# Kernel tuning notes

Hardware: AMD Instinct MI355X
Metric: run time of the kernel (lower is better)

The kernel has to match this reference:

```python
import jax, jax.numpy as jnp
import numpy as np

SMOOTH = 1.0
MAX_DIST = 10


def _neighbor_conv(x):
    # 3x3 ones kernel with zero center, padding=1 (NCHW, C=1)
    k = jnp.ones((1, 1, 3, 3), x.dtype).at[0, 0, 1, 1].set(0.0)
    return jax.lax.conv_general_dilated(
        x, k, window_strides=(1, 1), padding=[(1, 1), (1, 1)],
        dimension_numbers=('NCHW', 'OIHW', 'NCHW'))


def _analyze_skeleton(skel):
    n = _neighbor_conv(skel)
    on = skel > 0.5
    endpoints = ((n == 1) & on).astype(skel.dtype)
    midpoints = ((n == 2) & on).astype(skel.dtype)
    junctions = ((n > 2) & on).astype(skel.dtype)
    return endpoints, midpoints, junctions


def _iou(p, g):
    inter = jnp.sum(p * g, axis=(2, 3))
    union = jnp.sum(p, axis=(2, 3)) + jnp.sum(g, axis=(2, 3)) - inter
    return (inter + SMOOTH) / (union + SMOOTH)


def _structural_similarity(pred_skel, gt_skel):
    pe, pm, pj = _analyze_skeleton(pred_skel)
    ge, gm, gj = _analyze_skeleton(gt_skel)
    e_iou, m_iou, j_iou = _iou(pe, ge), _iou(pm, gm), _iou(pj, gj)
    ge_c = jnp.sum(ge, axis=(2, 3))
    gj_c = jnp.sum(gj, axis=(2, 3))
    gm_c = jnp.sum(gm, axis=(2, 3))
    total = ge_c + gj_c + gm_c + SMOOTH
    loss = 1.0 - ((ge_c / total) * e_iou + (gj_c / total) * j_iou + (gm_c / total) * m_iou)
    return loss.mean()


def _maxpool3(x):
    return jax.lax.reduce_window(
        x, -jnp.inf, jax.lax.max,
        window_dimensions=(1, 1, 3, 3), window_strides=(1, 1, 1, 1),
        padding=[(0, 0), (0, 0), (1, 1), (1, 1)])


def _distance_approximation(target, reference):
    # Fixed MAX_DIST iterations; identical math to the torch early-exit loop
    # because new_points requires ~found_mask (no distance is overwritten).
    tgt_on = target > 0.5

    def step(carry, d):
        dilated, found, dist = carry
        dilated = _maxpool3(dilated)
        new = (dilated > 0.5) & tgt_on & (~found)
        dist = dist + d.astype(dist.dtype) * new.astype(dist.dtype)
        return (dilated, found | new, dist), None

    init = (reference, jnp.zeros(target.shape, bool), jnp.zeros_like(target))
    (_, found, dist), _ = jax.lax.scan(step, init, jnp.arange(1, MAX_DIST + 1, dtype=jnp.int32))
    unfound = tgt_on & (~found)
    dist = dist + jnp.asarray(MAX_DIST, dist.dtype) * unfound.astype(dist.dtype)
    total_points = jnp.sum(tgt_on.astype(dist.dtype), axis=(2, 3))
    return jnp.sum(dist, axis=(2, 3)) / (total_points + SMOOTH)


def _medial_axis_distance(pred_skel, gt_skel):
    p2g = _distance_approximation(pred_skel, gt_skel)
    g2p = _distance_approximation(gt_skel, pred_skel)
    return (((p2g + g2p) / 2.0) / MAX_DIST).mean()


def setup_inputs() -> dict:
    key = jax.random.key(0)
    k1, k2 = jax.random.split(key)
    B, C, H, W = 32, 1, 512, 512
    pred_skel = jax.random.uniform(k1, (B, C, H, W), dtype=jnp.float32)
    gt_skel = (jax.random.uniform(k2, (B, C, H, W), dtype=jnp.float32) < 0.1).astype(jnp.float32)
    return {"pred_skel": pred_skel, "gt_skel": gt_skel}


def reference(pred_skel, gt_skel):
    inter = jnp.sum(pred_skel * gt_skel, axis=(2, 3))
    psum = jnp.sum(pred_skel, axis=(2, 3))
    gsum = jnp.sum(gt_skel, axis=(2, 3))
    dice = (2.0 * inter + SMOOTH) / (psum + gsum + SMOOTH)
    dice_loss = 1.0 - dice.mean()
    structural_loss = _structural_similarity(pred_skel, gt_skel)
    medial_loss = _medial_axis_distance(pred_skel, gt_skel)
    avg_mag = (dice_loss + structural_loss + medial_loss) / 3.0
    bal_dice = dice_loss / (dice_loss + SMOOTH) * avg_mag
    bal_struct = structural_loss / (structural_loss + SMOOTH) * avg_mag
    bal_medial = medial_loss / (medial_loss + SMOOTH) * avg_mag
    return bal_dice + bal_struct + bal_medial
```

## Files before the change

### kernel.cpp

```cpp
#include <hip/hip_runtime.h>
#include <stdint.h>

#define BATCH 32
#define H 512
#define W 512
#define NACC 16
#define TH 32
#define HALO 9
#define RH (TH + 2*HALO)
#define NWORDS (RH*8)
#define NT 1024
#define NW (NT/64)
#define NTILE (H/TH)
#define NBLK (NTILE*BATCH)


__global__ __launch_bounds__(NT, 4) void fused_kernel(
    const float* __restrict__ pred, const float* __restrict__ gt,
    float* __restrict__ part)
{
    __shared__ uint64_t MpS[NWORDS + 2];
    __shared__ uint64_t MgS[NWORDS + 2];
    __shared__ float    EC[2][TH];
    __shared__ float    redf[NW][2];
    __shared__ unsigned redu[NW][5];

    uint64_t* Mp = MpS + 1;
    uint64_t* Mg = MgS + 1;

    int fid  = blockIdx.x;
    int b    = fid & 31;
    int tile = fid >> 5;

    const float* pimg = pred + (size_t)b * H * W;
    const float* gimg = gt   + (size_t)b * H * W;
    int y0 = tile * TH;
    int tid = threadIdx.x, lane = tid & 63, wid = tid >> 6;

    float v0 = 0.f, v1 = 0.f;
    for (int s0 = wid; s0 < NWORDS; s0 += 4 * NW) {
        float vp[4], vg[4];
        #pragma unroll
        for (int u = 0; u < 4; ++u) {
            int s = s0 + u * NW;
            vp[u] = 0.f; vg[u] = 0.f;
            int ry = y0 - HALO + (s >> 3);
            if (s < NWORDS && (unsigned)ry < (unsigned)H) {
                int i0 = ry * W + (s & 7) * 64 + lane;
                vp[u] = pimg[i0]; vg[u] = gimg[i0];
            }
        }
        #pragma unroll
        for (int u = 0; u < 4; ++u) {
            int s = s0 + u * NW;
            if (s < NWORDS) {
                unsigned long long mp = __ballot(vp[u] > 0.5f);
                unsigned long long mg = __ballot(vg[u] > 0.5f);
                if (lane == 0) { Mp[s] = mp; Mg[s] = mg; }
                int r = s >> 3;
                if (r >= HALO && r < HALO + TH) {
                    v1 += vp[u];
                    v0 += (vg[u] > 0.5f) ? vp[u] : 0.f;
                }
            }
        }
    }
    if (tid == 0) { MpS[0] = 0; MpS[NWORDS + 1] = 0; MgS[0] = 0; MgS[NWORDS + 1] = 0; }

    bool isStencil = tid >= 512;
    int idx = tid & 511;
    int qi = idx & 127, h2 = idx >> 7;
    int x4 = qi * 4;
    int ys = y0 + h2 * 8;
    float4 pm4 = make_float4(0, 0, 0, 0), pc4 = make_float4(0, 0, 0, 0);
    if (isStencil) {
        if (ys > 0) pm4 = *(const float4*)(pimg + (size_t)(ys - 1) * W + x4);
        pc4 = *(const float4*)(pimg + (size_t)ys * W + x4);
    }

    if (tid < 2 * TH) {
        int c = tid >> 5, r = tid & (TH - 1);
        int y = y0 + r, col = 255 + c;
        float sum = (y > 0     ? pimg[(size_t)(y - 1) * W + col] : 0.f)
                  +              pimg[(size_t)y * W + col]
                  + (y < H - 1 ? pimg[(size_t)(y + 1) * W + col] : 0.f);
        EC[c][r] = sum;
    }
    __syncthreads();

    uint64_t cpack = 0ULL;
    int dsum = 0, dcnt = 0;

    if (isStencil) {
        int wdx = qi >> 4;
        int ss = (qi & 15) * 4;
        auto win6 = [&](int rb) -> uint32_t {
            const uint64_t* row = &Mg[rb * 8];
            uint64_t bm = row[wdx];
            if (ss == 0) {
                uint64_t lo = wdx ? row[wdx - 1] : 0ULL;
                return (uint32_t)(((bm << 1) | (lo >> 63)) & 0x3FULL);
            }
            uint32_t v = (uint32_t)((bm >> (ss - 1)) & 0x3FULL);
            if (ss == 60) {
                uint64_t hi = (wdx < 7) ? row[wdx + 1] : 0ULL;
                v |= ((uint32_t)hi & 1u) << 5;
            }
            return v;
        };
        int rb0 = h2 * 8 + HALO - 1;
        uint32_t wU = win6(rb0), wM = win6(rb0 + 1);

        for (int r = 0; r < 8; ++r) {
            int y = ys + r;
            float4 pp4 = (y < H - 1) ? *(const float4*)(pimg + (size_t)(y + 1) * W + x4)
                                     : make_float4(0, 0, 0, 0);
            uint32_t wD = win6(rb0 + 2 + r);
            int ry = h2 * 8 + r;

            float ps[6];
            ps[1] = pm4.x + pc4.x + pp4.x; ps[2] = pm4.y + pc4.y + pp4.y;
            ps[3] = pm4.z + pc4.z + pp4.z; ps[4] = pm4.w + pc4.w + pp4.w;
            float psl = __shfl_up(ps[4], 1, 64);
            float psr = __shfl_down(ps[1], 1, 64);
            if (lane == 0)  psl = (qi == 0)   ? 0.f : EC[0][ry];
            if (lane == 63) psr = (qi == 127) ? 0.f : EC[1][ry];
            ps[0] = psl; ps[5] = psr;

            float pcv[4] = {pc4.x, pc4.y, pc4.z, pc4.w};
            #pragma unroll
            for (int j = 0; j < 4; ++j) {
                float np = ps[j] + ps[j + 1] + ps[j + 2] - pcv[j];
                bool pon = pcv[j] > 0.5f;
                bool pe  = pon && (np == 1.f);
                bool pmb = pon && (np == 2.f);
                bool pjb = pon && (np > 2.f);
                uint32_t n9 = ((wU >> j) & 7u) | (((wM >> j) & 7u) << 3) | (((wD >> j) & 7u) << 6);
                uint32_t cen = (wM >> (j + 1)) & 1u;
                int ng = __popc(n9) - (int)cen;
                bool gon = cen != 0u;
                bool ge  = gon && (ng == 1);
                bool gmb = gon && (ng == 2);
                bool gjb = gon && (ng > 2);
                cpack += (uint64_t)pe
                       | ((uint64_t)pmb << 7)
                       | ((uint64_t)pjb << 14)
                       | ((uint64_t)ge  << 21)
                       | ((uint64_t)gmb << 28)
                       | ((uint64_t)gjb << 35)
                       | ((uint64_t)(pe  && ge)  << 42)
                       | ((uint64_t)(pmb && gmb) << 49)
                       | ((uint64_t)(pjb && gjb) << 56);
            }
            pm4 = pc4; pc4 = pp4; wU = wM; wM = wD;
        }
    } else {
        bool isP = tid < 256;
        int di = tid & 255;
        int o  = (HALO + (di >> 3)) * 8 + (di & 7);
        int w  = di & 7;
        bool wL = (w > 0), wR = (w < 7);
        const uint64_t* MT = isP ? Mp : Mg;
        const uint64_t* MV = isP ? Mg : Mp;

        uint64_t T = MT[o];
        dcnt = __popcll(T);
        dsum = dcnt;
        uint64_t VM = MV[o];
        uint64_t VL = wL ? MV[o - 1] : 0ULL;
        uint64_t VR = wR ? MV[o + 1] : 0ULL;
        uint64_t C = VM;

        #pragma unroll
        for (int a = 1; a <= 9; ++a) {
            int lo = o - 8 * a, hi = o + 8 * a;
            uint64_t NM = MV[lo] | MV[hi];
            uint64_t NL = wL ? (MV[lo - 1] | MV[hi - 1]) : 0ULL;
            uint64_t NR = wR ? (MV[lo + 1] | MV[hi + 1]) : 0ULL;
            uint64_t SL = NL, SM = NM, SR = NR;
            const int m = a - 1;
            if (m >= 1) {
                SM |= (SM << 1) | (SM >> 1) | (SL >> 63) | (SR << 63);
                SL |= SL << 1; SR |= SR >> 1;
            }
            if (m >= 2) {
                const int s = (m == 2) ? 1 : 2;
                SM |= (SM << s) | (SM >> s) | (SL >> (64 - s)) | (SR << (64 - s));
                SL |= SL << s; SR |= SR >> s;
            }
            if (m >= 4) {
                const int s = (m - 3 < 4) ? (m - 3) : 4;
                SM |= (SM << s) | (SM >> s) | (SL >> (64 - s)) | (SR << (64 - s));
                SL |= SL << s; SR |= SR >> s;
            }
            if (m >= 8) {
                const int s = m - 7;
                SM |= (SM << s) | (SM >> s) | (SL >> (64 - s)) | (SR << (64 - s));
                SL |= SL << s; SR |= SR >> s;
            }
            C |= SM;
            VL |= NL; VM |= NM; VR |= NR;
            C |= (VM << a) | (VM >> a) | (VL >> (64 - a)) | (VR << (64 - a));
            dsum += __popcll(T & ~C);
        }
    }

    unsigned r0, r1, r2, r3, r4;
    if (isStencil) {
        unsigned c3  = (unsigned)( cpack        & 0x7F);
        unsigned c4  = (unsigned)((cpack >> 7 ) & 0x7F);
        unsigned c5  = (unsigned)((cpack >> 14) & 0x7F);
        unsigned c6  = (unsigned)((cpack >> 21) & 0x7F);
        unsigned c7  = (unsigned)((cpack >> 28) & 0x7F);
        unsigned c8  = (unsigned)((cpack >> 35) & 0x7F);
        unsigned c9  = (unsigned)((cpack >> 42) & 0x7F);
        unsigned c10 = (unsigned)((cpack >> 49) & 0x7F);
        unsigned c11 = (unsigned)((cpack >> 56) & 0x7F);
        r0 = c3 | (c4 << 16); r1 = c5 | (c6 << 16); r2 = c7 | (c8 << 16);
        r3 = c9 | (c10 << 16); r4 = c11;
    } else {
        r0 = (unsigned)dsum | ((unsigned)dcnt << 16);
        r1 = 0; r2 = 0; r3 = 0; r4 = 0;
    }
    #pragma unroll
    for (int off = 32; off; off >>= 1) {
        v0 += __shfl_down(v0, off, 64);
        v1 += __shfl_down(v1, off, 64);
        r0 += __shfl_down(r0, off, 64);
        r1 += __shfl_down(r1, off, 64);
        r2 += __shfl_down(r2, off, 64);
        r3 += __shfl_down(r3, off, 64);
        r4 += __shfl_down(r4, off, 64);
    }
    if (lane == 0) {
        redf[wid][0] = v0; redf[wid][1] = v1;
        redu[wid][0] = r0; redu[wid][1] = r1; redu[wid][2] = r2;
        redu[wid][3] = r3; redu[wid][4] = r4;
    }
    __syncthreads();
    if (tid < 16) {
        int k = tid;
        float s = 0.f;
        if (k < 2) {
            #pragma unroll
            for (int wv = 0; wv < NW; ++wv) s += redf[wv][k];
        } else if (k == 2) {
            unsigned u = 0;
            for (int wv = 4; wv < 8; ++wv) u += redu[wv][0] >> 16;
            s = (float)u;
        } else if (k <= 10) {
            int pair = (k - 3) >> 1, hi = (k - 3) & 1;
            unsigned u = 0;
            for (int wv = 8; wv < 16; ++wv) u += (redu[wv][pair] >> (hi * 16)) & 0xFFFFu;
            s = (float)u;
        } else if (k == 11) {
            unsigned u = 0;
            for (int wv = 8; wv < 16; ++wv) u += redu[wv][4];
            s = (float)u;
        } else {
            int base = (k < 14) ? 0 : 4, hi = k & 1;
            unsigned u = 0;
            for (int wv = base; wv < base + 4; ++wv)
                u += (redu[wv][0] >> (hi * 16)) & 0xFFFFu;
            s = (float)u;
        }
        part[fid * NACC + k] = s;
    }
}

__global__ __launch_bounds__(512) void final_kernel(
    const float* __restrict__ part, float* __restrict__ out)
{
    __shared__ float sacc[BATCH][NACC];
    __shared__ float tri[BATCH][3];
    int t = threadIdx.x;
    {
        int b = t >> 4, k = t & 15;
        float s = 0.f;
        #pragma unroll 4
        for (int j = 0; j < NTILE; ++j)
            s += part[((j << 5) + b) * NACC + k];
        sacc[b][k] = s;
    }
    __syncthreads();
    if (t < BATCH) {
        const float* a = sacc[t];
        float inter = a[0], psum = a[1], gsum = a[2];
        float dice = (2.f * inter + 1.f) / (psum + gsum + 1.f);

        float pe = a[3], pm = a[4], pj = a[5];
        float ge = a[6], gm = a[7], gj = a[8];
        float ie = a[9], im = a[10], ij = a[11];
        float e_iou = (ie + 1.f) / (pe + ge - ie + 1.f);
        float m_iou = (im + 1.f) / (pm + gm - im + 1.f);
        float j_iou = (ij + 1.f) / (pj + gj - ij + 1.f);
        float total = ge + gj + gm + 1.f;
        float sloss = 1.f - ((ge / total) * e_iou + (gj / total) * j_iou + (gm / total) * m_iou);

        float p2g = a[12] / (a[13] + 1.f);
        float g2p = a[14] / (a[15] + 1.f);
        float med = ((p2g + g2p) * 0.5f) / 10.f;
        tri[t][0] = dice; tri[t][1] = sloss; tri[t][2] = med;
    }
    __syncthreads();
    if (t == 0) {
        float dice = 0.f, sloss = 0.f, med = 0.f;
        for (int b = 0; b < BATCH; ++b) {
            dice += tri[b][0]; sloss += tri[b][1]; med += tri[b][2];
        }
        float dice_loss  = 1.f - dice / (float)BATCH;
        float structural = sloss / (float)BATCH;
        float medial     = med / (float)BATCH;
        float avg = (dice_loss + structural + medial) / 3.f;
        float r = dice_loss  / (dice_loss  + 1.f) * avg
                + structural / (structural + 1.f) * avg
                + medial     / (medial     + 1.f) * avg;
        out[0] = r;
    }
}

extern "C" void kernel_launch(void* const* d_in, const int* in_sizes, int n_in,
                              void* d_out, int out_size, void* d_ws, size_t ws_size,
                              hipStream_t stream)
{
    const float* pred = (const float*)d_in[0];
    const float* gt   = (const float*)d_in[1];
    float* part = (float*)d_ws;
    float* out  = (float*)d_out;

    fused_kernel<<<dim3(NBLK), NT, 0, stream>>>(pred, gt, part);
    final_kernel<<<1, 512, 0, stream>>>(part, out);
}
```

Measured before the change: 118.8 us.

## Classify GT skeleton with bit-sliced popcount in LDS and early-exit distance loop

Computes the ground-truth endpoint/midpoint/junction masks once per tile using a bit-parallel carry-save adder over 64-bit packed rows, stores them in shared memory, and has stencil threads read single bits instead of recomputing per-pixel 3x3 popcounts. The GT counts move to the distance-threads' reduction slot, which cuts the packed reduction from five registers to three. The distance dilation loop now exits once a wavefront has no remaining unfound target bits. This adds shared memory and one extra barrier in exchange for less per-pixel integer work and fewer dilation iterations.

```diff
diff --git a/kernel.cpp b/kernel.cpp
--- a/kernel.cpp
+++ b/kernel.cpp
@@ -21,9 +21,12 @@
 {
     __shared__ uint64_t MpS[NWORDS + 2];
     __shared__ uint64_t MgS[NWORDS + 2];
+    __shared__ uint64_t Ge[TH * 8];
+    __shared__ uint64_t Gm[TH * 8];
+    __shared__ uint64_t Gj[TH * 8];
     __shared__ float    EC[2][TH];
     __shared__ float    redf[NW][2];
-    __shared__ unsigned redu[NW][5];
+    __shared__ unsigned redu[NW][3];
 
     uint64_t* Mp = MpS + 1;
     uint64_t* Mg = MgS + 1;
@@ -88,35 +91,53 @@
     }
     __syncthreads();
 
+    unsigned cge = 0, cgm = 0, cgj = 0;
+    if (tid < 256) {
+        int r = tid >> 3, w = tid & 7;
+        int oM = (HALO + r) * 8 + w;
+        bool wl = (w > 0), wr = (w < 7);
+        uint64_t A  = Mg[oM - 8], Bm = Mg[oM], Cm = Mg[oM + 8];
+        uint64_t AL = wl ? Mg[oM - 9] : 0ULL, AR = wr ? Mg[oM - 7] : 0ULL;
+        uint64_t BL = wl ? Mg[oM - 1] : 0ULL, BR = wr ? Mg[oM + 1] : 0ULL;
+        uint64_t CL = wl ? Mg[oM + 7] : 0ULL, CR = wr ? Mg[oM + 9] : 0ULL;
+        uint64_t Aw = (A  << 1) | (AL >> 63), Ae = (A  >> 1) | (AR << 63);
+        uint64_t Bw = (Bm << 1) | (BL >> 63), Be = (Bm >> 1) | (BR << 63);
+        uint64_t Cw = (Cm << 1) | (CL >> 63), Ce = (Cm >> 1) | (CR << 63);
+        uint64_t c1, c2, c3, c5;
+        uint64_t t;
+        t = Aw ^ A;  uint64_t s1 = t ^ Ae;  c1 = (Aw & A)  | (Ae & t);
+        t = Bw ^ Be; uint64_t s2 = t ^ Cw;  c2 = (Bw & Be) | (Cw & t);
+        t = Cm ^ Ce; uint64_t s3 = t ^ s1;  c3 = (Cm & Ce) | (s1 & t);
+        uint64_t b0 = s2 ^ s3, c4 = s2 & s3;
+        t = c1 ^ c2; uint64_t s5 = t ^ c3;  c5 = (c1 & c2) | (c3 & t);
+        uint64_t b1 = s5 ^ c4, c6 = s5 & c4;
+        uint64_t b2 = c5 ^ c6, b3 = c5 & c6;
+        uint64_t nz23 = ~(b2 | b3);
+        uint64_t ge = Bm & b0 & ~b1 & nz23;
+        uint64_t gm = Bm & b1 & ~b0 & nz23;
+        uint64_t gj = Bm & (b2 | b3 | (b1 & b0));
+        Ge[tid] = ge; Gm[tid] = gm; Gj[tid] = gj;
+        cge = (unsigned)__popcll(ge);
+        cgm = (unsigned)__popcll(gm);
+        cgj = (unsigned)__popcll(gj);
+    }
+    __syncthreads();
+
     uint64_t cpack = 0ULL;
     int dsum = 0, dcnt = 0;
 
     if (isStencil) {
         int wdx = qi >> 4;
         int ss = (qi & 15) * 4;
-        auto win6 = [&](int rb) -> uint32_t {
-            const uint64_t* row = &Mg[rb * 8];
-            uint64_t bm = row[wdx];
-            if (ss == 0) {
-                uint64_t lo = wdx ? row[wdx - 1] : 0ULL;
-                return (uint32_t)(((bm << 1) | (lo >> 63)) & 0x3FULL);
-            }
-            uint32_t v = (uint32_t)((bm >> (ss - 1)) & 0x3FULL);
-            if (ss == 60) {
-                uint64_t hi = (wdx < 7) ? row[wdx + 1] : 0ULL;
-                v |= ((uint32_t)hi & 1u) << 5;
-            }
-            return v;
-        };
-        int rb0 = h2 * 8 + HALO - 1;
-        uint32_t wU = win6(rb0), wM = win6(rb0 + 1);
 
         for (int r = 0; r < 8; ++r) {
             int y = ys + r;
             float4 pp4 = (y < H - 1) ? *(const float4*)(pimg + (size_t)(y + 1) * W + x4)
                                      : make_float4(0, 0, 0, 0);
-            uint32_t wD = win6(rb0 + 2 + r);
             int ry = h2 * 8 + r;
+            uint64_t gew = Ge[ry * 8 + wdx];
+            uint64_t gmw = Gm[ry * 8 + wdx];
+            uint64_t gjw = Gj[ry * 8 + wdx];
 
             float ps[6];
             ps[1] = pm4.x + pc4.x + pp4.x; ps[2] = pm4.y + pc4.y + pp4.y;
@@ -135,24 +156,17 @@
                 bool pe  = pon && (np == 1.f);
                 bool pmb = pon && (np == 2.f);
                 bool pjb = pon && (np > 2.f);
-                uint32_t n9 = ((wU >> j) & 7u) | (((wM >> j) & 7u) << 3) | (((wD >> j) & 7u) << 6);
-                uint32_t cen = (wM >> (j + 1)) & 1u;
-                int ng = __popc(n9) - (int)cen;
-                bool gon = cen != 0u;
-                bool ge  = gon && (ng == 1);
-                bool gmb = gon && (ng == 2);
-                bool gjb = gon && (ng > 2);
+                unsigned geb = (unsigned)(gew >> (ss + j)) & 1u;
+                unsigned gmb = (unsigned)(gmw >> (ss + j)) & 1u;
+                unsigned gjb = (unsigned)(gjw >> (ss + j)) & 1u;
                 cpack += (uint64_t)pe
                        | ((uint64_t)pmb << 7)
                        | ((uint64_t)pjb << 14)
-                       | ((uint64_t)ge  << 21)
-                       | ((uint64_t)gmb << 28)
-                       | ((uint64_t)gjb << 35)
-                       | ((uint64_t)(pe  && ge)  << 42)
-                       | ((uint64_t)(pmb && gmb) << 49)
-                       | ((uint64_t)(pjb && gjb) << 56);
-            }
-            pm4 = pc4; pc4 = pp4; wU = wM; wM = wD;
+                       | ((uint64_t)(pe  && geb) << 21)
+                       | ((uint64_t)(pmb && gmb) << 28)
+                       | ((uint64_t)(pjb && gjb) << 35);
+            }
+            pm4 = pc4; pc4 = pp4;
         }
     } else {
         bool isP = tid < 256;
@@ -201,26 +215,25 @@
             C |= SM;
             VL |= NL; VM |= NM; VR |= NR;
             C |= (VM << a) | (VM >> a) | (VL >> (64 - a)) | (VR << (64 - a));
-            dsum += __popcll(T & ~C);
-        }
-    }
-
-    unsigned r0, r1, r2, r3, r4;
+            uint64_t rem = T & ~C;
+            dsum += __popcll(rem);
+            if (__all(rem == 0ULL)) break;
+        }
+    }
+
+    unsigned r0, r1, r2;
     if (isStencil) {
-        unsigned c3  = (unsigned)( cpack        & 0x7F);
-        unsigned c4  = (unsigned)((cpack >> 7 ) & 0x7F);
-        unsigned c5  = (unsigned)((cpack >> 14) & 0x7F);
-        unsigned c6  = (unsigned)((cpack >> 21) & 0x7F);
-        unsigned c7  = (unsigned)((cpack >> 28) & 0x7F);
-        unsigned c8  = (unsigned)((cpack >> 35) & 0x7F);
-        unsigned c9  = (unsigned)((cpack >> 42) & 0x7F);
-        unsigned c10 = (unsigned)((cpack >> 49) & 0x7F);
-        unsigned c11 = (unsigned)((cpack >> 56) & 0x7F);
-        r0 = c3 | (c4 << 16); r1 = c5 | (c6 << 16); r2 = c7 | (c8 << 16);
-        r3 = c9 | (c10 << 16); r4 = c11;
+        unsigned c_pe = (unsigned)( cpack        & 0x7F);
+        unsigned c_pm = (unsigned)((cpack >> 7 ) & 0x7F);
+        unsigned c_pj = (unsigned)((cpack >> 14) & 0x7F);
+        unsigned c_ie = (unsigned)((cpack >> 21) & 0x7F);
+        unsigned c_im = (unsigned)((cpack >> 28) & 0x7F);
+        unsigned c_ij = (unsigned)((cpack >> 35) & 0x7F);
+        r0 = c_pe | (c_pm << 16); r1 = c_pj | (c_ie << 16); r2 = c_im | (c_ij << 16);
     } else {
         r0 = (unsigned)dsum | ((unsigned)dcnt << 16);
-        r1 = 0; r2 = 0; r3 = 0; r4 = 0;
+        r1 = cge | (cgm << 16);
+        r2 = cgj;
     }
     #pragma unroll
     for (int off = 32; off; off >>= 1) {
@@ -229,13 +242,10 @@
         r0 += __shfl_down(r0, off, 64);
         r1 += __shfl_down(r1, off, 64);
         r2 += __shfl_down(r2, off, 64);
-        r3 += __shfl_down(r3, off, 64);
-        r4 += __shfl_down(r4, off, 64);
     }
     if (lane == 0) {
         redf[wid][0] = v0; redf[wid][1] = v1;
         redu[wid][0] = r0; redu[wid][1] = r1; redu[wid][2] = r2;
-        redu[wid][3] = r3; redu[wid][4] = r4;
     }
     __syncthreads();
     if (tid < 16) {
@@ -244,24 +254,14 @@
         if (k < 2) {
             #pragma unroll
             for (int wv = 0; wv < NW; ++wv) s += redf[wv][k];
-        } else if (k == 2) {
+        } else {
+            static const uint8_t WB[16] = {0,0, 4, 8,8,8, 0,0,0, 8,8,8, 0,0,4,4};
+            static const uint8_t WC[16] = {0,0, 4, 8,8,8, 4,4,4, 8,8,8, 4,4,4,4};
+            static const uint8_t RG[16] = {0,0, 0, 0,0,1, 1,1,2, 1,2,2, 0,0,0,0};
+            static const uint8_t HI[16] = {0,0, 1, 0,1,0, 0,1,0, 1,0,1, 0,1,0,1};
             unsigned u = 0;
-            for (int wv = 4; wv < 8; ++wv) u += redu[wv][0] >> 16;
-            s = (float)u;
-        } else if (k <= 10) {
-            int pair = (k - 3) >> 1, hi = (k - 3) & 1;
-            unsigned u = 0;
-            for (int wv = 8; wv < 16; ++wv) u += (redu[wv][pair] >> (hi * 16)) & 0xFFFFu;
-            s = (float)u;
-        } else if (k == 11) {
-            unsigned u = 0;
-            for (int wv = 8; wv < 16; ++wv) u += redu[wv][4];
-            s = (float)u;
-        } else {
-            int base = (k < 14) ? 0 : 4, hi = k & 1;
-            unsigned u = 0;
-            for (int wv = base; wv < base + 4; ++wv)
-                u += (redu[wv][0] >> (hi * 16)) & 0xFFFFu;
+            for (int wv = WB[k]; wv < WB[k] + WC[k]; ++wv)
+                u += (redu[wv][RG[k]] >> (HI[k] * 16)) & 0xFFFFu;
             s = (float)u;
         }
         part[fid * NACC + k] = s;
```

Measured after the change: 112.0 us. 5.7% less time.
